# Kernel optimization log

Hardware: AMD Instinct MI355X
Metric: run time of the kernel (lower is better)

The kernel has to match this reference:

```python
import jax, jax.numpy as jnp
import numpy as np

NUM_NODES = 100000
E = 512    # embedding_size
U = 64     # embedding_u_size
T = 8      # edge_type_count
A = 32     # dim_a
B = 8192   # batch
NB = 10    # neighbors per type


def setup_inputs() -> dict:
    key = jax.random.key(0)
    ks = jax.random.split(key, 8)
    std = 1.0 / np.sqrt(E)
    return {
        "node_embeddings": jax.random.uniform(ks[0], (NUM_NODES, E), jnp.float32, -1.0, 1.0),
        "node_type_embeddings": jax.random.uniform(ks[1], (NUM_NODES, T, U), jnp.float32, -1.0, 1.0),
        "trans_weights": jax.random.normal(ks[2], (T, U, E), jnp.float32) * std,
        "trans_weights_s1": jax.random.normal(ks[3], (T, U, A), jnp.float32) * std,
        "trans_weights_s2": jax.random.normal(ks[4], (T, A, 1), jnp.float32) * std,
        "train_inputs": jax.random.randint(ks[5], (B,), 0, NUM_NODES, jnp.int32),
        "train_types": jax.random.randint(ks[6], (B,), 0, T, jnp.int32),
        "node_neigh": jax.random.randint(ks[7], (B, T, NB), 0, NUM_NODES, jnp.int32),
    }


def reference(node_embeddings, node_type_embeddings, trans_weights,
              trans_weights_s1, trans_weights_s2,
              train_inputs, train_types, node_neigh):
    # node_embed: [B, E]
    node_embed = node_embeddings[train_inputs]
    # Per-type neighbor gather. Original materializes [B,T,NB,T,U] then takes the
    # diagonal over the two type axes; we gather only the diagonal directly:
    # neigh_embed[b,t,n,:] = node_type_embeddings[node_neigh[b,t,n], t, :]
    type_idx = jnp.arange(T)[None, :, None]              # [1,T,1]
    neigh_embed = node_type_embeddings[node_neigh, type_idx]  # [B,T,NB,U]
    node_type_embed = neigh_embed.sum(axis=2)            # [B,T,U]

    # Per-sample gathered projection weights (MoE-style by edge type)
    w_s1 = trans_weights_s1[train_types]                 # [B,U,A]
    w_s2 = trans_weights_s2[train_types]                 # [B,A,1]
    w = trans_weights[train_types]                       # [B,U,E]

    # attention over edge types
    h = jnp.tanh(jnp.einsum('btu,bua->bta', node_type_embed, w_s1))  # [B,T,A]
    scores = jnp.einsum('bta,bao->bt', h, w_s2)          # [B,T] (squeeze of [B,T,1])
    attention = jax.nn.softmax(scores, axis=-1)          # [B,T]

    agg = jnp.einsum('bt,btu->bu', attention, node_type_embed)  # [B,U]
    node_embed = node_embed + jnp.einsum('bu,bue->be', agg, w)  # [B,E]

    # F.normalize(dim=1): divide by L2 norm clamped at 1e-12
    norm = jnp.maximum(jnp.linalg.norm(node_embed, axis=1, keepdims=True), 1e-12)
    return node_embed / norm
```

## Files before the change

### kernel.cpp

```cpp
#include <hip/hip_runtime.h>

#define E_DIM 512
#define U_DIM 64
#define T_DIM 8
#define A_DIM 32
#define NB    10
#define BATCH 8192
#define BKT_STRIDE 8192


__global__ __launch_bounds__(256) void bucket_kernel(
    const int* __restrict__ types, int* __restrict__ cnt, int* __restrict__ bkt)
{
    const int i = blockIdx.x * 256 + threadIdx.x;
    const int ty = types[i];
    const unsigned long long below = (1ull << (threadIdx.x & 63)) - 1;
    #pragma unroll
    for (int t = 0; t < T_DIM; ++t) {
        unsigned long long m = __ballot(ty == t);
        if (ty == t) {
            int lead = __ffsll(m) - 1;
            int base = 0;
            if ((threadIdx.x & 63) == lead)
                base = atomicAdd(&cnt[t], (int)__popcll(m));
            base = __shfl(base, lead, 64);
            bkt[t * BKT_STRIDE + base + (int)__popcll(m & below)] = i;
        }
    }
}

static __device__ __forceinline__ float bcast_lane(float x, int l) {
    return __int_as_float(__builtin_amdgcn_readlane(__float_as_int(x), l));
}

__global__ __launch_bounds__(256) void gatne_main(
    const float* __restrict__ node_embeddings,
    const float* __restrict__ node_type_embeddings,
    const float* __restrict__ trans_weights,
    const float* __restrict__ trans_weights_s1,
    const float* __restrict__ trans_weights_s2,
    const int*   __restrict__ train_inputs,
    const int*   __restrict__ counts,
    const int*   __restrict__ bkt,
    const int*   __restrict__ node_neigh,
    float*       __restrict__ out)
{
    const int ty    = blockIdx.x;
    const int count = counts[ty];
    if ((int)(blockIdx.y * 4) >= count) return;

    const int tid  = threadIdx.x;
    const int lane = tid & 63;
    const int w    = tid >> 6;

    __shared__ __align__(16) float sW1T[A_DIM * 68];
    __shared__ __align__(16) float sNte[4][T_DIM * 68];
    __shared__ __align__(16) float sSc[4][8];
    __shared__ float sW2[A_DIM];
    __shared__ int   sNei[4][80];

    for (int k = tid; k < U_DIM * A_DIM; k += 256) {
        const int u = k >> 5, a = k & 31;
        sW1T[a * 68 + u] = trans_weights_s1[ty * (U_DIM * A_DIM) + k];
    }
    if (tid < A_DIM) sW2[tid] = trans_weights_s2[ty * A_DIM + tid];
    __syncthreads();

    const float* Wty = trans_weights + (size_t)ty * (U_DIM * E_DIM);
    const int t8 = lane >> 3;
    const int a0 = lane & 7;

    for (int j = blockIdx.y; j * 4 < count; j += gridDim.y) {
        const int  si    = j * 4 + w;
        const bool valid = si < count;
        float agg = 0.f;
        int s = 0, ni = 0;

        if (valid) {
            s  = bkt[ty * BKT_STRIDE + si];
            ni = train_inputs[s];
            {
                const int* np = node_neigh + (size_t)s * (T_DIM * NB);
                sNei[w][lane] = np[lane];
                if (lane < 16) sNei[w][64 + lane] = np[64 + lane];
            }
            float acc[T_DIM];
            #pragma unroll
            for (int t = 0; t < T_DIM; ++t) {
                float a = 0.f;
                #pragma unroll
                for (int n = 0; n < NB; ++n) {
                    const int nb = sNei[w][t * NB + n];
                    a += node_type_embeddings[(size_t)nb * (T_DIM * U_DIM) + t * U_DIM + lane];
                }
                acc[t] = a;
                sNte[w][t * 68 + lane] = a;
            }
            float h0 = 0.f, h1 = 0.f, h2 = 0.f, h3 = 0.f;
            #pragma unroll
            for (int uq = 0; uq < 16; ++uq) {
                const float4 nv  = *(const float4*)&sNte[w][t8 * 68 + uq * 4];
                const float4 wa  = *(const float4*)&sW1T[(a0     ) * 68 + uq * 4];
                const float4 wb  = *(const float4*)&sW1T[(a0 +  8) * 68 + uq * 4];
                const float4 wc  = *(const float4*)&sW1T[(a0 + 16) * 68 + uq * 4];
                const float4 wd  = *(const float4*)&sW1T[(a0 + 24) * 68 + uq * 4];
                h0 = fmaf(nv.x, wa.x, h0); h0 = fmaf(nv.y, wa.y, h0);
                h0 = fmaf(nv.z, wa.z, h0); h0 = fmaf(nv.w, wa.w, h0);
                h1 = fmaf(nv.x, wb.x, h1); h1 = fmaf(nv.y, wb.y, h1);
                h1 = fmaf(nv.z, wb.z, h1); h1 = fmaf(nv.w, wb.w, h1);
                h2 = fmaf(nv.x, wc.x, h2); h2 = fmaf(nv.y, wc.y, h2);
                h2 = fmaf(nv.z, wc.z, h2); h2 = fmaf(nv.w, wc.w, h2);
                h3 = fmaf(nv.x, wd.x, h3); h3 = fmaf(nv.y, wd.y, h3);
                h3 = fmaf(nv.z, wd.z, h3); h3 = fmaf(nv.w, wd.w, h3);
            }
            float r = tanhf(h0) * sW2[a0]      + tanhf(h1) * sW2[a0 + 8]
                    + tanhf(h2) * sW2[a0 + 16] + tanhf(h3) * sW2[a0 + 24];
            r += __shfl_xor(r, 1, 64);
            r += __shfl_xor(r, 2, 64);
            r += __shfl_xor(r, 4, 64);
            if (a0 == 0) sSc[w][t8] = r;
            const float4 sc0 = *(const float4*)&sSc[w][0];
            const float4 sc1 = *(const float4*)&sSc[w][4];
            float mx = fmaxf(fmaxf(fmaxf(sc0.x, sc0.y), fmaxf(sc0.z, sc0.w)),
                             fmaxf(fmaxf(sc1.x, sc1.y), fmaxf(sc1.z, sc1.w)));
            const float e0 = __expf(sc0.x - mx), e1 = __expf(sc0.y - mx);
            const float e2 = __expf(sc0.z - mx), e3 = __expf(sc0.w - mx);
            const float e4 = __expf(sc1.x - mx), e5 = __expf(sc1.y - mx);
            const float e6 = __expf(sc1.z - mx), e7 = __expf(sc1.w - mx);
            const float inv = 1.f / (e0 + e1 + e2 + e3 + e4 + e5 + e6 + e7);
            agg = (e0 * acc[0] + e1 * acc[1] + e2 * acc[2] + e3 * acc[3]
                 + e4 * acc[4] + e5 * acc[5] + e6 * acc[6] + e7 * acc[7]) * inv;
        }

        __syncthreads();

        if (valid) {
            float v[8];
            const float4* nr = (const float4*)(node_embeddings + (size_t)ni * E_DIM + lane * 8);
            const float4 nv0 = nr[0], nv1 = nr[1];
            v[0] = nv0.x; v[1] = nv0.y; v[2] = nv0.z; v[3] = nv0.w;
            v[4] = nv1.x; v[5] = nv1.y; v[6] = nv1.z; v[7] = nv1.w;
            const float* Wp = Wty + lane * 8;
            #pragma unroll 8
            for (int u = 0; u < U_DIM; ++u) {
                const float au = bcast_lane(agg, u);
                const float4 w0 = *(const float4*)(Wp + (size_t)u * E_DIM);
                const float4 w1 = *(const float4*)(Wp + (size_t)u * E_DIM + 4);
                v[0] = fmaf(au, w0.x, v[0]); v[1] = fmaf(au, w0.y, v[1]);
                v[2] = fmaf(au, w0.z, v[2]); v[3] = fmaf(au, w0.w, v[3]);
                v[4] = fmaf(au, w1.x, v[4]); v[5] = fmaf(au, w1.y, v[5]);
                v[6] = fmaf(au, w1.z, v[6]); v[7] = fmaf(au, w1.w, v[7]);
            }
            float ss = v[0]*v[0] + v[1]*v[1] + v[2]*v[2] + v[3]*v[3]
                     + v[4]*v[4] + v[5]*v[5] + v[6]*v[6] + v[7]*v[7];
            #pragma unroll
            for (int off = 1; off < 64; off <<= 1)
                ss += __shfl_xor(ss, off, 64);
            const float invn = 1.f / fmaxf(sqrtf(ss), 1e-12f);
            float4 o0, o1;
            o0.x = v[0]*invn; o0.y = v[1]*invn; o0.z = v[2]*invn; o0.w = v[3]*invn;
            o1.x = v[4]*invn; o1.y = v[5]*invn; o1.z = v[6]*invn; o1.w = v[7]*invn;
            float4* op = (float4*)(out + (size_t)s * E_DIM + lane * 8);
            op[0] = o0; op[1] = o1;
        }
    }
}

extern "C" void kernel_launch(void* const* d_in, const int* in_sizes, int n_in,
                              void* d_out, int out_size, void* d_ws, size_t ws_size,
                              hipStream_t stream) {
    const float* node_embeddings      = (const float*)d_in[0];
    const float* node_type_embeddings = (const float*)d_in[1];
    const float* trans_weights        = (const float*)d_in[2];
    const float* trans_weights_s1     = (const float*)d_in[3];
    const float* trans_weights_s2     = (const float*)d_in[4];
    const int*   train_inputs         = (const int*)d_in[5];
    const int*   train_types          = (const int*)d_in[6];
    const int*   node_neigh           = (const int*)d_in[7];
    float* out = (float*)d_out;

    int* cnt = (int*)d_ws;
    int* bkt = (int*)((char*)d_ws + 256);

    hipMemsetAsync(cnt, 0, 32, stream);
    bucket_kernel<<<BATCH / 256, 256, 0, stream>>>(train_types, cnt, bkt);
    gatne_main<<<dim3(T_DIM, 128), 256, 0, stream>>>(
        node_embeddings, node_type_embeddings, trans_weights,
        trans_weights_s1, trans_weights_s2,
        train_inputs, cnt, bkt, node_neigh, out);
}
```

Baseline: 430.2 us.

## Process four samples per wavefront to reuse projection weight loads

Each wavefront now handles a group of four samples of the same edge type. It computes their attention aggregates in turn, then runs one projection loop in which each loaded row of the type weight matrix is applied to all four samples. The block-wide barrier between phases is removed and the grid y-dimension is halved. This is meant to cut global weight traffic per sample by four. In exchange it raises register pressure (32 accumulators plus four aggregates per lane), leaves fewer waves to hide gather latency, and serialises the per-sample gathers inside each wave.

```diff
diff --git a/kernel.cpp b/kernel.cpp
--- a/kernel.cpp
+++ b/kernel.cpp
@@ -47,11 +47,9 @@
 {
     const int ty    = blockIdx.x;
     const int count = counts[ty];
-    if ((int)(blockIdx.y * 4) >= count) return;
-
-    const int tid  = threadIdx.x;
-    const int lane = tid & 63;
-    const int w    = tid >> 6;
+    const int tid   = threadIdx.x;
+    const int lane  = tid & 63;
+    const int w     = tid >> 6;
 
     __shared__ __align__(16) float sW1T[A_DIM * 68];
     __shared__ __align__(16) float sNte[4][T_DIM * 68];
@@ -70,15 +68,19 @@
     const int t8 = lane >> 3;
     const int a0 = lane & 7;
 
-    for (int j = blockIdx.y; j * 4 < count; j += gridDim.y) {
-        const int  si    = j * 4 + w;
-        const bool valid = si < count;
-        float agg = 0.f;
-        int s = 0, ni = 0;
-
-        if (valid) {
-            s  = bkt[ty * BKT_STRIDE + si];
-            ni = train_inputs[s];
+    const int wstride = gridDim.y * 4;
+    for (int g = blockIdx.y * 4 + w; g * 4 < count; g += wstride) {
+        const int nvalid = min(4, count - g * 4);
+        int   sidx[4], nidx[4];
+        float agg[4];
+
+        #pragma unroll
+        for (int i = 0; i < 4; ++i) {
+            agg[i] = 0.f; sidx[i] = 0; nidx[i] = 0;
+            if (i >= nvalid) continue;
+            const int s = bkt[ty * BKT_STRIDE + g * 4 + i];
+            sidx[i] = s;
+            nidx[i] = train_inputs[s];
             {
                 const int* np = node_neigh + (size_t)s * (T_DIM * NB);
                 sNei[w][lane] = np[lane];
@@ -99,11 +101,11 @@
             float h0 = 0.f, h1 = 0.f, h2 = 0.f, h3 = 0.f;
             #pragma unroll
             for (int uq = 0; uq < 16; ++uq) {
-                const float4 nv  = *(const float4*)&sNte[w][t8 * 68 + uq * 4];
-                const float4 wa  = *(const float4*)&sW1T[(a0     ) * 68 + uq * 4];
-                const float4 wb  = *(const float4*)&sW1T[(a0 +  8) * 68 + uq * 4];
-                const float4 wc  = *(const float4*)&sW1T[(a0 + 16) * 68 + uq * 4];
-                const float4 wd  = *(const float4*)&sW1T[(a0 + 24) * 68 + uq * 4];
+                const float4 nv = *(const float4*)&sNte[w][t8 * 68 + uq * 4];
+                const float4 wa = *(const float4*)&sW1T[(a0     ) * 68 + uq * 4];
+                const float4 wb = *(const float4*)&sW1T[(a0 +  8) * 68 + uq * 4];
+                const float4 wc = *(const float4*)&sW1T[(a0 + 16) * 68 + uq * 4];
+                const float4 wd = *(const float4*)&sW1T[(a0 + 24) * 68 + uq * 4];
                 h0 = fmaf(nv.x, wa.x, h0); h0 = fmaf(nv.y, wa.y, h0);
                 h0 = fmaf(nv.z, wa.z, h0); h0 = fmaf(nv.w, wa.w, h0);
                 h1 = fmaf(nv.x, wb.x, h1); h1 = fmaf(nv.y, wb.y, h1);
@@ -128,39 +130,53 @@
             const float e4 = __expf(sc1.x - mx), e5 = __expf(sc1.y - mx);
             const float e6 = __expf(sc1.z - mx), e7 = __expf(sc1.w - mx);
             const float inv = 1.f / (e0 + e1 + e2 + e3 + e4 + e5 + e6 + e7);
-            agg = (e0 * acc[0] + e1 * acc[1] + e2 * acc[2] + e3 * acc[3]
-                 + e4 * acc[4] + e5 * acc[5] + e6 * acc[6] + e7 * acc[7]) * inv;
-        }
-
-        __syncthreads();
-
-        if (valid) {
-            float v[8];
-            const float4* nr = (const float4*)(node_embeddings + (size_t)ni * E_DIM + lane * 8);
-            const float4 nv0 = nr[0], nv1 = nr[1];
-            v[0] = nv0.x; v[1] = nv0.y; v[2] = nv0.z; v[3] = nv0.w;
-            v[4] = nv1.x; v[5] = nv1.y; v[6] = nv1.z; v[7] = nv1.w;
-            const float* Wp = Wty + lane * 8;
-            #pragma unroll 8
-            for (int u = 0; u < U_DIM; ++u) {
-                const float au = bcast_lane(agg, u);
-                const float4 w0 = *(const float4*)(Wp + (size_t)u * E_DIM);
-                const float4 w1 = *(const float4*)(Wp + (size_t)u * E_DIM + 4);
-                v[0] = fmaf(au, w0.x, v[0]); v[1] = fmaf(au, w0.y, v[1]);
-                v[2] = fmaf(au, w0.z, v[2]); v[3] = fmaf(au, w0.w, v[3]);
-                v[4] = fmaf(au, w1.x, v[4]); v[5] = fmaf(au, w1.y, v[5]);
-                v[6] = fmaf(au, w1.z, v[6]); v[7] = fmaf(au, w1.w, v[7]);
-            }
-            float ss = v[0]*v[0] + v[1]*v[1] + v[2]*v[2] + v[3]*v[3]
-                     + v[4]*v[4] + v[5]*v[5] + v[6]*v[6] + v[7]*v[7];
+            agg[i] = (e0 * acc[0] + e1 * acc[1] + e2 * acc[2] + e3 * acc[3]
+                    + e4 * acc[4] + e5 * acc[5] + e6 * acc[6] + e7 * acc[7]) * inv;
+        }
+
+        float v[4][8];
+        #pragma unroll
+        for (int i = 0; i < 4; ++i) {
+            if (i < nvalid) {
+                const float4* nr = (const float4*)(node_embeddings
+                                     + (size_t)nidx[i] * E_DIM + lane * 8);
+                const float4 n0 = nr[0], n1 = nr[1];
+                v[i][0] = n0.x; v[i][1] = n0.y; v[i][2] = n0.z; v[i][3] = n0.w;
+                v[i][4] = n1.x; v[i][5] = n1.y; v[i][6] = n1.z; v[i][7] = n1.w;
+            } else {
+                #pragma unroll
+                for (int k = 0; k < 8; ++k) v[i][k] = 0.f;
+            }
+        }
+        const float* Wp = Wty + lane * 8;
+        #pragma unroll 8
+        for (int u = 0; u < U_DIM; ++u) {
+            const float4 w0 = *(const float4*)(Wp + (size_t)u * E_DIM);
+            const float4 w1 = *(const float4*)(Wp + (size_t)u * E_DIM + 4);
+            #pragma unroll
+            for (int i = 0; i < 4; ++i) {
+                const float au = bcast_lane(agg[i], u);
+                v[i][0] = fmaf(au, w0.x, v[i][0]); v[i][1] = fmaf(au, w0.y, v[i][1]);
+                v[i][2] = fmaf(au, w0.z, v[i][2]); v[i][3] = fmaf(au, w0.w, v[i][3]);
+                v[i][4] = fmaf(au, w1.x, v[i][4]); v[i][5] = fmaf(au, w1.y, v[i][5]);
+                v[i][6] = fmaf(au, w1.z, v[i][6]); v[i][7] = fmaf(au, w1.w, v[i][7]);
+            }
+        }
+        #pragma unroll
+        for (int i = 0; i < 4; ++i) {
+            if (i >= nvalid) continue;
+            float ss = v[i][0]*v[i][0] + v[i][1]*v[i][1] + v[i][2]*v[i][2] + v[i][3]*v[i][3]
+                     + v[i][4]*v[i][4] + v[i][5]*v[i][5] + v[i][6]*v[i][6] + v[i][7]*v[i][7];
             #pragma unroll
             for (int off = 1; off < 64; off <<= 1)
                 ss += __shfl_xor(ss, off, 64);
             const float invn = 1.f / fmaxf(sqrtf(ss), 1e-12f);
             float4 o0, o1;
-            o0.x = v[0]*invn; o0.y = v[1]*invn; o0.z = v[2]*invn; o0.w = v[3]*invn;
-            o1.x = v[4]*invn; o1.y = v[5]*invn; o1.z = v[6]*invn; o1.w = v[7]*invn;
-            float4* op = (float4*)(out + (size_t)s * E_DIM + lane * 8);
+            o0.x = v[i][0]*invn; o0.y = v[i][1]*invn;
+            o0.z = v[i][2]*invn; o0.w = v[i][3]*invn;
+            o1.x = v[i][4]*invn; o1.y = v[i][5]*invn;
+            o1.z = v[i][6]*invn; o1.w = v[i][7]*invn;
+            float4* op = (float4*)(out + (size_t)sidx[i] * E_DIM + lane * 8);
             op[0] = o0; op[1] = o1;
         }
     }
@@ -184,7 +200,7 @@
 
     hipMemsetAsync(cnt, 0, 32, stream);
     bucket_kernel<<<BATCH / 256, 256, 0, stream>>>(train_types, cnt, bkt);
-    gatne_main<<<dim3(T_DIM, 128), 256, 0, stream>>>(
+    gatne_main<<<dim3(T_DIM, 64), 256, 0, stream>>>(
         node_embeddings, node_type_embeddings, trans_weights,
         trans_weights_s1, trans_weights_s2,
         train_inputs, cnt, bkt, node_neigh, out);
```

Result: faster. 416.9 us (-3.1%).
